# Performance work log

Measured on AMD Instinct MI355X. Metric: run time of the kernel, lower is better.

Reference implementation:

```python
import jax, jax.numpy as jnp
import numpy as np

KNOW, ITEM, D, L, LAT, B, S = 1024, 20000, 128, 2, 256, 256, 200
NTOT = ITEM + KNOW
E1, E2 = 32768, 160000


def graph_layer(h, W, a, src, dst, n):
    # GAT-style: gather src/dst, edge MLP, segment softmax over dst, weighted scatter-sum
    z = h @ W                                              # [N, D]
    e = jax.nn.leaky_relu((jnp.concatenate([z[src], z[dst]], axis=-1) @ a)[:, 0])  # [E]
    m = jax.ops.segment_max(e, dst, num_segments=n)
    m = jnp.where(jnp.isfinite(m), m, 0.0)                 # nodes with no in-edges
    w = jnp.exp(e - m[dst])                                # [E]
    den = jax.ops.segment_sum(w, dst, num_segments=n)      # [N]
    num = jax.ops.segment_sum(w[:, None] * z[src], dst, num_segments=n)  # [N, D]
    return jnp.where(den[:, None] > 0, num / jnp.maximum(den, 1e-12)[:, None], 0.0)


def setup_inputs() -> dict:
    key = jax.random.key(0)
    ks = jax.random.split(key, 32)
    p = lambda i, shp: jax.random.normal(ks[i], shp, dtype=jnp.float32) * 0.05
    inp = {
        'p_rec': jax.random.randint(ks[0], (B, S), 0, ITEM),
        'p_target': jax.random.randint(ks[1], (B,), 0, S),
        'a_rec': jax.random.randint(ks[2], (B, S), 0, 3),
        'kn_rec': jax.random.uniform(ks[3], (B, S, KNOW), dtype=jnp.float32),
        'kn_num': jnp.ones((B, S), dtype=jnp.float32),
        'src1': jax.random.randint(ks[4], (E1,), 0, KNOW),
        'dst1': jax.random.randint(ks[5], (E1,), 0, KNOW),
        'src2': jax.random.randint(ks[6], (E2,), 0, NTOT),
        'dst2': jax.random.randint(ks[7], (E2,), 0, NTOT),
        'src3': jax.random.randint(ks[8], (E2,), 0, NTOT),
        'dst3': jax.random.randint(ks[9], (E2,), 0, NTOT),
        'kn_table': p(10, (KNOW, D)),
        'exer_table': p(11, (ITEM, D)),
        'ans_table': p(12, (3, D)),
        'gW': p(13, (L, 3, D, D)),
        'gA': p(14, (L, 3, 2 * D, 1)),
        'raW1': p(15, (L, D, D)),
        'raB1': jnp.zeros((L, D), jnp.float32),
        'raW2': p(16, (L, D, 1)),
        'actW1': p(17, (3 * D, LAT)),
        'actB1': jnp.zeros((LAT,), jnp.float32),
        'actW2': p(18, (LAT, ITEM)),
        'actB2': jnp.zeros((ITEM,), jnp.float32),
        'vW1': p(19, (3, 3 * D, LAT)),
        'vB1': jnp.zeros((3, LAT), jnp.float32),
        'vW2': p(20, (3, LAT, 1)),
        'vB2': jnp.zeros((3, 1), jnp.float32),
    }
    return inp


def reference(p_rec, p_target, a_rec, kn_rec, kn_num, src1, dst1, src2, dst2, src3, dst3,
              kn_table, exer_table, ans_table, gW, gA, raW1, raB1, raW2,
              actW1, actB1, actW2, actB2, vW1, vB1, vW2, vB2):
    kn, ex = kn_table, exer_table
    for l in range(L):  # GraphEncoder: stacked Fusion blocks (distinct params)
        k_dir = graph_layer(kn, gW[l, 0], gA[l, 0], src1, dst1, KNOW)
        ek = jnp.concatenate([ex, kn], axis=0)             # [NTOT, D]
        kfe = graph_layer(ek, gW[l, 1], gA[l, 1], src2, dst2, NTOT)
        efk = graph_layer(ek, gW[l, 2], gA[l, 2], src3, dst3, NTOT)
        A_, B_ = k_dir, kfe[ITEM:]
        ra = lambda x: jnp.tanh(x @ raW1[l] + raB1[l]) @ raW2[l]  # [KNOW, 1]
        s = jax.nn.softmax(jnp.concatenate([ra(A_), ra(B_)], axis=1), axis=1)
        kn = s[:, :1] * A_ + s[:, 1:2] * B_
        ex = efk[:ITEM]
    # hidden_layer
    be = ex[p_rec]                                         # [B, S, D]
    ba = ans_table[a_rec]                                  # [B, S, D]
    bk = jnp.einsum('bsk,kd->bsd', kn_rec, kn) / kn_num[..., None]
    item = jnp.concatenate([be, ba, bk], axis=-1)          # [B, S, 3D]
    m = (jnp.arange(S)[None, :] < (p_target + 1)[:, None]).astype(item.dtype)
    h = (item * m[..., None]).sum(axis=1) / m.sum(axis=1, keepdims=True)  # [B, 3D]
    logits = jnp.tanh(h @ actW1 + actB1) @ actW2 + actB2   # [B, ITEM]
    vh = jnp.tanh(jnp.einsum('bd,kdl->kbl', h, vW1) + vB1[:, None, :])
    vals = jnp.einsum('kbl,klo->kbo', vh, vW2) + vB2[:, None, :]  # [3, B, 1]
    return logits, vals[0], vals[1], vals[2]
```

## Files before the change

kernel.cpp:

```cpp
#include <hip/hip_runtime.h>

#define D 128
#define KNOW 1024
#define ITEM 20000
#define NTOT (ITEM + KNOW)
#define LAYERS 2
#define LAT 256
#define BB 256
#define SS 200
#define H3 (3 * D)
#define ZROWS 64
#define NBK (KNOW / ZROWS)
#define NBN ((NTOT + ZROWS - 1) / ZROWS)
#define XPITCH 68

__global__ __launch_bounds__(256) void zdv(
    const float* __restrict__ Xe, const float* __restrict__ Xk,
    const float* __restrict__ gW, const float* __restrict__ gA, int layer,
    float* __restrict__ z1, float* __restrict__ z2, float* __restrict__ z3,
    float* __restrict__ ds1, float* __restrict__ dd1,
    float* __restrict__ ds2, float* __restrict__ dd2,
    float* __restrict__ ds3, float* __restrict__ dd3)
{
    __shared__ __align__(16) float xT[D * XPITCH];
    int bid = blockIdx.x;
    int g, row0, nmax;
    if (bid < NBK)            { g = 0; row0 = bid * ZROWS;                nmax = KNOW; }
    else if (bid < NBK + NBN) { g = 1; row0 = (bid - NBK) * ZROWS;        nmax = NTOT; }
    else                      { g = 2; row0 = (bid - NBK - NBN) * ZROWS;  nmax = NTOT; }
    const float* W = gW + (size_t)(layer * 3 + g) * D * D;
    const float* A = gA + (size_t)(layer * 3 + g) * 2 * D;
    float* Z  = (g == 0) ? z1  : (g == 1 ? z2  : z3);
    float* DS = (g == 0) ? ds1 : (g == 1 ? ds2 : ds3);
    float* DD = (g == 0) ? dd1 : (g == 1 ? dd2 : dd3);

    int tid = threadIdx.x;
#pragma unroll
    for (int i = 0; i < 8; ++i) {
        int flat = tid + i * 256;
        int row  = flat >> 5;
        int f4   = flat & 31;
        int grow = row0 + row;
        float4 v = make_float4(0.f, 0.f, 0.f, 0.f);
        if (grow < nmax) {
            const float* src = (g == 0) ? (Xk + (size_t)grow * D)
                             : (grow < ITEM ? Xe + (size_t)grow * D
                                            : Xk + (size_t)(grow - ITEM) * D);
            v = *(const float4*)(src + f4 * 4);
        }
        int slot = row ^ ((f4 & 7) << 2);
        int kk = f4 * 4;
        xT[(kk + 0) * XPITCH + slot] = v.x;
        xT[(kk + 1) * XPITCH + slot] = v.y;
        xT[(kk + 2) * XPITCH + slot] = v.z;
        xT[(kk + 3) * XPITCH + slot] = v.w;
    }
    __syncthreads();

    int cg = tid & 31;
    int rg = tid >> 5;
    int c0 = cg * 4;
    int r0a = rg * 8, r0b = rg * 8 + 4;

    float acc[8][4];
#pragma unroll
    for (int r = 0; r < 8; ++r)
#pragma unroll
        for (int c = 0; c < 4; ++c) acc[r][c] = 0.f;

#pragma unroll 4
    for (int k = 0; k < D; ++k) {
        float4 wv = *(const float4*)(W + (size_t)k * D + c0);
        int xc = ((k >> 2) & 7) << 2;
        float4 xa = *(const float4*)&xT[k * XPITCH + (r0a ^ xc)];
        float4 xb = *(const float4*)&xT[k * XPITCH + (r0b ^ xc)];
        acc[0][0] = fmaf(xa.x, wv.x, acc[0][0]); acc[0][1] = fmaf(xa.x, wv.y, acc[0][1]);
        acc[0][2] = fmaf(xa.x, wv.z, acc[0][2]); acc[0][3] = fmaf(xa.x, wv.w, acc[0][3]);
        acc[1][0] = fmaf(xa.y, wv.x, acc[1][0]); acc[1][1] = fmaf(xa.y, wv.y, acc[1][1]);
        acc[1][2] = fmaf(xa.y, wv.z, acc[1][2]); acc[1][3] = fmaf(xa.y, wv.w, acc[1][3]);
        acc[2][0] = fmaf(xa.z, wv.x, acc[2][0]); acc[2][1] = fmaf(xa.z, wv.y, acc[2][1]);
        acc[2][2] = fmaf(xa.z, wv.z, acc[2][2]); acc[2][3] = fmaf(xa.z, wv.w, acc[2][3]);
        acc[3][0] = fmaf(xa.w, wv.x, acc[3][0]); acc[3][1] = fmaf(xa.w, wv.y, acc[3][1]);
        acc[3][2] = fmaf(xa.w, wv.z, acc[3][2]); acc[3][3] = fmaf(xa.w, wv.w, acc[3][3]);
        acc[4][0] = fmaf(xb.x, wv.x, acc[4][0]); acc[4][1] = fmaf(xb.x, wv.y, acc[4][1]);
        acc[4][2] = fmaf(xb.x, wv.z, acc[4][2]); acc[4][3] = fmaf(xb.x, wv.w, acc[4][3]);
        acc[5][0] = fmaf(xb.y, wv.x, acc[5][0]); acc[5][1] = fmaf(xb.y, wv.y, acc[5][1]);
        acc[5][2] = fmaf(xb.y, wv.z, acc[5][2]); acc[5][3] = fmaf(xb.y, wv.w, acc[5][3]);
        acc[6][0] = fmaf(xb.z, wv.x, acc[6][0]); acc[6][1] = fmaf(xb.z, wv.y, acc[6][1]);
        acc[6][2] = fmaf(xb.z, wv.z, acc[6][2]); acc[6][3] = fmaf(xb.z, wv.w, acc[6][3]);
        acc[7][0] = fmaf(xb.w, wv.x, acc[7][0]); acc[7][1] = fmaf(xb.w, wv.y, acc[7][1]);
        acc[7][2] = fmaf(xb.w, wv.z, acc[7][2]); acc[7][3] = fmaf(xb.w, wv.w, acc[7][3]);
    }

#pragma unroll
    for (int r = 0; r < 8; ++r) {
        int grow = row0 + ((r < 4) ? (r0a + r) : (r0b + r - 4));
        if (grow < nmax) {
            float4 v = make_float4(acc[r][0], acc[r][1], acc[r][2], acc[r][3]);
            *(float4*)(Z + (size_t)grow * D + c0) = v;
        }
    }

    float4 as = *(const float4*)(A + c0);
    float4 ad = *(const float4*)(A + D + c0);
    float ps[8], pd[8];
#pragma unroll
    for (int r = 0; r < 8; ++r) {
        ps[r] = acc[r][0] * as.x + acc[r][1] * as.y + acc[r][2] * as.z + acc[r][3] * as.w;
        pd[r] = acc[r][0] * ad.x + acc[r][1] * ad.y + acc[r][2] * ad.z + acc[r][3] * ad.w;
    }
#pragma unroll
    for (int m = 16; m; m >>= 1) {
#pragma unroll
        for (int r = 0; r < 8; ++r) {
            ps[r] += __shfl_xor(ps[r], m, 64);
            pd[r] += __shfl_xor(pd[r], m, 64);
        }
    }
    if (cg == 0) {
#pragma unroll
        for (int r = 0; r < 8; ++r) {
            int grow = row0 + ((r < 4) ? (r0a + r) : (r0b + r - 4));
            if (grow < nmax) { DS[grow] = ps[r]; DD[grow] = pd[r]; }
        }
    }
}

__global__ void hist3(const int* __restrict__ d1, const int* __restrict__ d2, const int* __restrict__ d3,
                      int E1, int E2, int* __restrict__ c1, int* __restrict__ c2, int* __restrict__ c3) {
    int i = blockIdx.x * blockDim.x + threadIdx.x;
    if (i < E1) atomicAdd(&c1[d1[i]], 1);
    else if (i < E1 + E2) { int d = d2[i - E1]; if (d >= ITEM) atomicAdd(&c2[d - ITEM], 1); }
    else if (i < E1 + 2 * E2) { int d = d3[i - E1 - E2]; if (d < ITEM) atomicAdd(&c3[d], 1); }
}

__global__ __launch_bounds__(1024) void exscan3(int* __restrict__ c1, int* __restrict__ o1,
                                                int* __restrict__ c2, int* __restrict__ o2,
                                                int* __restrict__ c3, int* __restrict__ o3) {
    int g = blockIdx.x;
    int* cnt = (g == 0) ? c1 : (g == 1 ? c2 : c3);
    int* off = (g == 0) ? o1 : (g == 1 ? o2 : o3);
    int n = (g == 2) ? ITEM : KNOW;
    int tid = threadIdx.x, lane = tid & 63, wid = tid >> 6;
    int L = (n + 1023) >> 10;
    int i0 = tid * L;
    int sum = 0;
    for (int q = 0; q < L; ++q) {
        int i = i0 + q;
        if (i < n) sum += cnt[i];
    }
    int x = sum;
#pragma unroll
    for (int d = 1; d < 64; d <<= 1) { int t = __shfl_up(x, d, 64); if (lane >= d) x += t; }
    __shared__ int ws[16];
    if (lane == 63) ws[wid] = x;
    __syncthreads();
    if (wid == 0) {
        int w = (lane < 16) ? ws[lane] : 0;
#pragma unroll
        for (int d = 1; d < 16; d <<= 1) { int t = __shfl_up(w, d, 64); if (lane >= d) w += t; }
        if (lane < 16) ws[lane] = w;
    }
    __syncthreads();
    int run = x - sum + ((wid > 0) ? ws[wid - 1] : 0);
    if (tid == 0) off[0] = 0;
    for (int q = 0; q < L; ++q) {
        int i = i0 + q;
        if (i < n) {
            int v = cnt[i];
            cnt[i] = run;
            run += v;
            off[i + 1] = run;
        }
    }
}

__global__ void scatter3(const int* __restrict__ s1, const int* __restrict__ d1,
                         const int* __restrict__ s2, const int* __restrict__ d2,
                         const int* __restrict__ s3, const int* __restrict__ d3,
                         int E1, int E2, int* __restrict__ cur1, int* __restrict__ cur2, int* __restrict__ cur3,
                         int* __restrict__ e1, int* __restrict__ e2, int* __restrict__ e3) {
    int i = blockIdx.x * blockDim.x + threadIdx.x;
    if (i < E1) { int p = atomicAdd(&cur1[d1[i]], 1); e1[p] = s1[i]; }
    else if (i < E1 + E2) { int j = i - E1; int d = d2[j]; if (d >= ITEM) { int p = atomicAdd(&cur2[d - ITEM], 1); e2[p] = s2[j]; } }
    else if (i < E1 + 2 * E2) { int j = i - E1 - E2; int d = d3[j]; if (d < ITEM) { int p = atomicAdd(&cur3[d], 1); e3[p] = s3[j]; } }
}

__device__ __forceinline__ void agg_row(const float* __restrict__ Z, const float* __restrict__ dsrc,
                                        float dd, const int* __restrict__ es, int e0, int e1,
                                        int lane, float* __restrict__ acc) {
#pragma unroll
    for (int q = 0; q < 8; ++q) acc[q] = 0.f;
    if (e1 <= e0) return;
    float mx = -3.4e38f;
    for (int e = e0 + lane; e < e1; e += 64) {
        float t = dsrc[es[e]] + dd;
        t = (t > 0.f) ? t : 0.01f * t;
        mx = fmaxf(mx, t);
    }
#pragma unroll
    for (int o = 32; o; o >>= 1) mx = fmaxf(mx, __shfl_xor(mx, o, 64));
    int eg = lane >> 4, cs = lane & 15;
    float den = 0.f;
    for (int e = e0 + eg; e < e1; e += 4) {
        int s = es[e];
        float t = dsrc[s] + dd;
        t = (t > 0.f) ? t : 0.01f * t;
        float w = __expf(t - mx);
        den += w;
        const float4* zr = (const float4*)(Z + (size_t)s * D + cs * 8);
        float4 za = zr[0], zb = zr[1];
        acc[0] = fmaf(w, za.x, acc[0]); acc[1] = fmaf(w, za.y, acc[1]);
        acc[2] = fmaf(w, za.z, acc[2]); acc[3] = fmaf(w, za.w, acc[3]);
        acc[4] = fmaf(w, zb.x, acc[4]); acc[5] = fmaf(w, zb.y, acc[5]);
        acc[6] = fmaf(w, zb.z, acc[6]); acc[7] = fmaf(w, zb.w, acc[7]);
    }
#pragma unroll
    for (int m = 16; m <= 32; m <<= 1) {
        den += __shfl_xor(den, m, 64);
#pragma unroll
        for (int q = 0; q < 8; ++q) acc[q] += __shfl_xor(acc[q], m, 64);
    }
    float inv = 1.f / fmaxf(den, 1e-12f);
#pragma unroll
    for (int q = 0; q < 8; ++q) acc[q] *= inv;
}

__global__ __launch_bounds__(256) void agg3c(
    const float* __restrict__ z1, const float* __restrict__ z2, const float* __restrict__ z3,
    const float* __restrict__ ds1, const float* __restrict__ dd1,
    const float* __restrict__ ds2, const float* __restrict__ dd2,
    const float* __restrict__ ds3, const float* __restrict__ dd3,
    const int* __restrict__ off1, const int* __restrict__ es1,
    const int* __restrict__ off2, const int* __restrict__ es2,
    const int* __restrict__ off3, const int* __restrict__ es3,
    const float* __restrict__ raW1, const float* __restrict__ raB1,
    const float* __restrict__ raW2, float* __restrict__ buf)
{
    int wv = threadIdx.x >> 6, lane = threadIdx.x & 63;
    int eg = lane >> 4, cs = lane & 15;
    if (blockIdx.x < KNOW / 4) {
        __shared__ float ABs[4][2][D];
        int i = blockIdx.x * 4 + wv;
        float accA[8], accB[8];
        agg_row(z1, ds1, dd1[i], es1, off1[i], off1[i + 1], lane, accA);
        agg_row(z2, ds2, dd2[ITEM + i], es2, off2[i], off2[i + 1], lane, accB);
        if (eg == 0) {
            *(float4*)&ABs[wv][0][cs * 8]     = make_float4(accA[0], accA[1], accA[2], accA[3]);
            *(float4*)&ABs[wv][0][cs * 8 + 4] = make_float4(accA[4], accA[5], accA[6], accA[7]);
            *(float4*)&ABs[wv][1][cs * 8]     = make_float4(accB[0], accB[1], accB[2], accB[3]);
            *(float4*)&ABs[wv][1][cs * 8 + 4] = make_float4(accB[4], accB[5], accB[6], accB[7]);
        }
        __syncthreads();
        int j0 = lane * 2;
        float b0 = raB1[j0], b1 = raB1[j0 + 1];
        float aA0 = b0, aA1 = b1, aB0 = b0, aB1 = b1;
#pragma unroll 4
        for (int k = 0; k < D; ++k) {
            float av = ABs[wv][0][k], bv = ABs[wv][1][k];
            float2 w = *(const float2*)(raW1 + (size_t)k * D + j0);
            aA0 = fmaf(av, w.x, aA0); aA1 = fmaf(av, w.y, aA1);
            aB0 = fmaf(bv, w.x, aB0); aB1 = fmaf(bv, w.y, aB1);
        }
        float2 w2 = *(const float2*)(raW2 + j0);
        float pA = tanhf(aA0) * w2.x + tanhf(aA1) * w2.y;
        float pB = tanhf(aB0) * w2.x + tanhf(aB1) * w2.y;
#pragma unroll
        for (int o = 32; o; o >>= 1) { pA += __shfl_xor(pA, o, 64); pB += __shfl_xor(pB, o, 64); }
        float mx2 = fmaxf(pA, pB);
        float eA = __expf(pA - mx2), eB = __expf(pB - mx2);
        float s = 1.f / (eA + eB);
        float sA = eA * s, sB = eB * s;
        float2 Av = *(float2*)&ABs[wv][0][j0];
        float2 Bv = *(float2*)&ABs[wv][1][j0];
        *(float2*)(buf + (size_t)(ITEM + i) * D + j0) =
            make_float2(sA * Av.x + sB * Bv.x, sA * Av.y + sB * Bv.y);
    } else {
        int row = (blockIdx.x - KNOW / 4) * 4 + wv;
        if (row < ITEM) {
            float acc[8];
            agg_row(z3, ds3, dd3[row], es3, off3[row], off3[row + 1], lane, acc);
            if (eg == 0) {
                *(float4*)(buf + (size_t)row * D + cs * 8)     = make_float4(acc[0], acc[1], acc[2], acc[3]);
                *(float4*)(buf + (size_t)row * D + cs * 8 + 4) = make_float4(acc[4], acc[5], acc[6], acc[7]);
            }
        }
    }
}

__global__ __launch_bounds__(512) void hker(const float* __restrict__ ex, const float* __restrict__ ans_table,
                                            const int* __restrict__ p_rec, const int* __restrict__ a_rec,
                                            const int* __restrict__ p_target,
                                            const float* __restrict__ kn_rec, const float* __restrict__ kn_num,
                                            const float* __restrict__ kn, float* __restrict__ h) {
    int b = blockIdx.x;
    int tid = threadIdx.x;
    int j = tid & 127, sg = tid >> 7;
    int cnt = p_target[b] + 1;
    __shared__ int pidx[SS], aidx[SS];
    __shared__ float kr[KNOW];
    __shared__ float red[4][3][128];
    for (int i = tid; i < cnt; i += 512) { pidx[i] = p_rec[b * SS + i]; aidx[i] = a_rec[b * SS + i]; }
    {
        float a0 = 0.f, a1 = 0.f;
        const float* kb = kn_rec + (size_t)b * SS * KNOW + tid * 2;
        const float* nb = kn_num + (size_t)b * SS;
#pragma unroll 2
        for (int s = 0; s < cnt; ++s) {
            float inv = 1.f / nb[s];
            float2 v = *(const float2*)(kb + (size_t)s * KNOW);
            a0 = fmaf(v.x, inv, a0); a1 = fmaf(v.y, inv, a1);
        }
        kr[tid * 2] = a0; kr[tid * 2 + 1] = a1;
    }
    __syncthreads();
    float accE = 0.f, accA = 0.f;
    for (int s = sg; s < cnt; s += 4) {
        accE += ex[(size_t)pidx[s] * D + j];
        accA += ans_table[aidx[s] * D + j];
    }
    float accK = 0.f;
    for (int k = sg * 256; k < sg * 256 + 256; ++k) accK += kr[k] * kn[(size_t)k * D + j];
    red[sg][0][j] = accE; red[sg][1][j] = accA; red[sg][2][j] = accK;
    __syncthreads();
    if (sg == 0) {
        float inv = 1.f / (float)cnt;
        float e = (red[0][0][j] + red[1][0][j] + red[2][0][j] + red[3][0][j]) * inv;
        float a = (red[0][1][j] + red[1][1][j] + red[2][1][j] + red[3][1][j]) * inv;
        float kv = (red[0][2][j] + red[1][2][j] + red[2][2][j] + red[3][2][j]) * inv;
        h[b * H3 + j] = e;
        h[b * H3 + D + j] = a;
        h[b * H3 + 2 * D + j] = kv;
    }
}

__global__ __launch_bounds__(256) void hidden_gemm(const float* __restrict__ h,
                                                   const float* __restrict__ actW1, const float* __restrict__ actB1,
                                                   const float* __restrict__ vW1, const float* __restrict__ vB1,
                                                   float* __restrict__ hid) {
    __shared__ float hT[H3 * 17];
    int tid = threadIdx.x;
    int b0 = blockIdx.y * 16;
    for (int idx = tid; idx < 16 * H3; idx += 256) {
        int r = idx / H3, k = idx - r * H3;
        hT[k * 17 + r] = h[(size_t)(b0 + r) * H3 + k];
    }
    __syncthreads();
    int j = blockIdx.x * 64 + (tid & 63);
    int head = j >> 8, jj = j & 255;
    int rg = tid >> 6, r0 = rg * 4;
    const float* W = (head == 0) ? actW1 : (vW1 + (size_t)(head - 1) * H3 * LAT);
    float bias = (head == 0) ? actB1[jj] : vB1[(head - 1) * LAT + jj];
    float acc[4] = {bias, bias, bias, bias};
#pragma unroll 4
    for (int k = 0; k < H3; ++k) {
        float w = W[(size_t)k * LAT + jj];
        float h0 = hT[k * 17 + r0 + 0];
        float h1 = hT[k * 17 + r0 + 1];
        float h2 = hT[k * 17 + r0 + 2];
        float h3 = hT[k * 17 + r0 + 3];
        acc[0] = fmaf(h0, w, acc[0]);
        acc[1] = fmaf(h1, w, acc[1]);
        acc[2] = fmaf(h2, w, acc[2]);
        acc[3] = fmaf(h3, w, acc[3]);
    }
#pragma unroll
    for (int r = 0; r < 4; ++r)
        hid[((size_t)head * BB + (b0 + r0 + r)) * LAT + jj] = tanhf(acc[r]);
}

__global__ __launch_bounds__(256) void logitsker(const float* __restrict__ hid, const float* __restrict__ actW2,
                                                 const float* __restrict__ actB2, float* __restrict__ out) {
    __shared__ float hT[LAT * 33];
    int tid = threadIdx.x;
    int b0 = blockIdx.y * 32;
    for (int idx = tid; idx < 32 * LAT; idx += 256) {
        int r = idx >> 8, k = idx & 255;
        hT[k * 33 + r] = hid[(size_t)(b0 + r) * LAT + k];
    }
    __syncthreads();
    int lane6 = tid & 63;
    int rg = tid >> 6, r0 = rg * 8;
    int ibase = blockIdx.x * 256 + lane6;
    int icol[4], icl[4];
    float bias[4];
#pragma unroll
    for (int c = 0; c < 4; ++c) {
        icol[c] = ibase + c * 64;
        icl[c] = icol[c] < ITEM ? icol[c] : (ITEM - 1);
        bias[c] = actB2[icl[c]];
    }
    float acc[8][4];
#pragma unroll
    for (int r = 0; r < 8; ++r)
#pragma unroll
        for (int c = 0; c < 4; ++c) acc[r][c] = bias[c];
#pragma unroll 2
    for (int k = 0; k < LAT; ++k) {
        float w0 = actW2[(size_t)k * ITEM + icl[0]];
        float w1 = actW2[(size_t)k * ITEM + icl[1]];
        float w2 = actW2[(size_t)k * ITEM + icl[2]];
        float w3 = actW2[(size_t)k * ITEM + icl[3]];
        const float* hp = &hT[k * 33 + r0];
#pragma unroll
        for (int r = 0; r < 8; ++r) {
            float hv = hp[r];
            acc[r][0] = fmaf(hv, w0, acc[r][0]);
            acc[r][1] = fmaf(hv, w1, acc[r][1]);
            acc[r][2] = fmaf(hv, w2, acc[r][2]);
            acc[r][3] = fmaf(hv, w3, acc[r][3]);
        }
    }
#pragma unroll
    for (int c = 0; c < 4; ++c) {
        if (icol[c] < ITEM) {
#pragma unroll
            for (int r = 0; r < 8; ++r)
                out[(size_t)(b0 + r0 + r) * ITEM + icol[c]] = acc[r][c];
        }
    }
}

__global__ __launch_bounds__(256) void valsker(const float* __restrict__ hid, const float* __restrict__ vW2,
                                               const float* __restrict__ vB2, float* __restrict__ out) {
    int idx = blockIdx.x * 4 + (threadIdx.x >> 6);
    int lane = threadIdx.x & 63;
    if (idx >= 3 * BB) return;
    int k = idx / BB, b = idx - k * BB;
    const float* vh = hid + ((size_t)(k + 1) * BB + b) * LAT;
    float4 a = ((const float4*)vh)[lane];
    float4 w = ((const float4*)(vW2 + k * LAT))[lane];
    float s = a.x * w.x + a.y * w.y + a.z * w.z + a.w * w.w;
#pragma unroll
    for (int o = 32; o; o >>= 1) s += __shfl_down(s, o, 64);
    if (lane == 0) out[(size_t)BB * ITEM + k * BB + b] = s + vB2[k];
}

extern "C" void kernel_launch(void* const* d_in, const int* in_sizes, int n_in,
                              void* d_out, int out_size, void* d_ws, size_t ws_size,
                              hipStream_t stream) {
    const int*   p_rec      = (const int*)d_in[0];
    const int*   p_target   = (const int*)d_in[1];
    const int*   a_rec      = (const int*)d_in[2];
    const float* kn_rec     = (const float*)d_in[3];
    const float* kn_num     = (const float*)d_in[4];
    const int*   src1       = (const int*)d_in[5];
    const int*   dst1       = (const int*)d_in[6];
    const int*   src2       = (const int*)d_in[7];
    const int*   dst2       = (const int*)d_in[8];
    const int*   src3       = (const int*)d_in[9];
    const int*   dst3       = (const int*)d_in[10];
    const float* kn_table   = (const float*)d_in[11];
    const float* exer_table = (const float*)d_in[12];
    const float* ans_table  = (const float*)d_in[13];
    const float* gW         = (const float*)d_in[14];
    const float* gA         = (const float*)d_in[15];
    const float* raW1       = (const float*)d_in[16];
    const float* raB1       = (const float*)d_in[17];
    const float* raW2       = (const float*)d_in[18];
    const float* actW1      = (const float*)d_in[19];
    const float* actB1      = (const float*)d_in[20];
    const float* actW2      = (const float*)d_in[21];
    const float* actB2      = (const float*)d_in[22];
    const float* vW1        = (const float*)d_in[23];
    const float* vB1        = (const float*)d_in[24];
    const float* vW2        = (const float*)d_in[25];
    const float* vB2        = (const float*)d_in[26];
    const int E1 = in_sizes[5], E2 = in_sizes[7];

    float* base = (float*)d_ws;
    size_t o = 0;
    auto alloc = [&](size_t n) -> float* { float* p = base + o; o += (n + 3) & ~(size_t)3; return p; };
    float* buf  = alloc((size_t)NTOT * D);
    float* z1   = alloc((size_t)KNOW * D);
    float* z2   = alloc((size_t)NTOT * D);
    float* z3   = alloc((size_t)NTOT * D);
    float* ds1 = alloc(KNOW);  float* dd1 = alloc(KNOW);
    float* ds2 = alloc(NTOT);  float* dd2 = alloc(NTOT);
    float* ds3 = alloc(NTOT);  float* dd3 = alloc(NTOT);
    int* cnts = (int*)alloc(2 * KNOW + NTOT);
    int* cnt1 = cnts, *cnt2 = cnts + KNOW, *cnt3 = cnts + 2 * KNOW;
    int* off1 = (int*)alloc(KNOW + 1);
    int* off2 = (int*)alloc(KNOW + 1);
    int* off3 = (int*)alloc(ITEM + 1);
    int* es1  = (int*)alloc(E1);
    int* es2  = (int*)alloc(E2);
    int* es3  = (int*)alloc(E2);
    float* hbuf  = alloc((size_t)BB * H3);
    float* hid   = alloc((size_t)4 * BB * LAT);

    hipMemsetAsync(cnts, 0, sizeof(int) * (2 * KNOW + NTOT), stream);

    int etot = E1 + 2 * E2;
    hist3<<<(etot + 255) / 256, 256, 0, stream>>>(dst1, dst2, dst3, E1, E2, cnt1, cnt2, cnt3);
    exscan3<<<3, 1024, 0, stream>>>(cnt1, off1, cnt2, off2, cnt3, off3);
    scatter3<<<(etot + 255) / 256, 256, 0, stream>>>(src1, dst1, src2, dst2, src3, dst3,
                                                     E1, E2, cnt1, cnt2, cnt3, es1, es2, es3);

    int aggBlocks = KNOW / 4 + ITEM / 4;
    for (int l = 0; l < LAYERS; ++l) {
        const float* Xe = (l == 0) ? exer_table : buf;
        const float* Xk = (l == 0) ? kn_table : (buf + (size_t)ITEM * D);
        zdv<<<NBK + 2 * NBN, 256, 0, stream>>>(Xe, Xk, gW, gA, l, z1, z2, z3,
                                               ds1, dd1, ds2, dd2, ds3, dd3);
        agg3c<<<aggBlocks, 256, 0, stream>>>(z1, z2, z3, ds1, dd1, ds2, dd2, ds3, dd3,
                                             off1, es1, off2, es2, off3, es3,
                                             raW1 + (size_t)l * D * D, raB1 + (size_t)l * D,
                                             raW2 + (size_t)l * D, buf);
    }

    hker<<<BB, 512, 0, stream>>>(buf, ans_table, p_rec, a_rec, p_target, kn_rec, kn_num,
                                 buf + (size_t)ITEM * D, hbuf);
    hidden_gemm<<<dim3(16, 16), 256, 0, stream>>>(hbuf, actW1, actB1, vW1, vB1, hid);
    logitsker<<<dim3((ITEM + 255) / 256, 8), 256, 0, stream>>>(hid, actW2, actB2, (float*)d_out);
    valsker<<<(3 * BB + 3) / 4, 256, 0, stream>>>(hid, vW2, vB2, (float*)d_out);
}
```

Baseline: 320.9 us.

## Split kn_rec row reduction over sequence chunks into separate kernel

Moves the masked sum of kn_rec/kn_num over the sequence out of hker into a new krowk kernel. krowk runs a BB x CH grid, each block summing one chunk of the sequence with float4 loads and writing a partial row. hker then adds the CH partials. The old loop ran 256 blocks serially over up to 200 rows of the ~200MB kn_rec, so the goal is more memory-level parallelism for that stream, at the cost of an extra launch and 8MB of partial-sum traffic.

```diff
diff --git a/kernel.cpp b/kernel.cpp
--- a/kernel.cpp
+++ b/kernel.cpp
@@ -9,6 +9,7 @@
 #define BB 256
 #define SS 200
 #define H3 (3 * D)
+#define CH 8
 #define ZROWS 64
 #define NBK (KNOW / ZROWS)
 #define NBN ((NTOT + ZROWS - 1) / ZROWS)
@@ -288,30 +289,39 @@
     }
 }
 
+__global__ __launch_bounds__(256) void krowk(const float* __restrict__ kn_rec, const float* __restrict__ kn_num,
+                                             const int* __restrict__ p_target, float* __restrict__ krowP) {
+    int b = blockIdx.x, ch = blockIdx.y;
+    int cnt = p_target[b] + 1;
+    int per = (SS + CH - 1) / CH;
+    int s0 = ch * per, s1 = s0 + per;
+    if (s1 > cnt) s1 = cnt;
+    int k0 = threadIdx.x * 4;
+    float4 a = make_float4(0.f, 0.f, 0.f, 0.f);
+    for (int s = s0; s < s1; ++s) {
+        float inv = 1.f / kn_num[b * SS + s];
+        float4 v = *(const float4*)(kn_rec + ((size_t)b * SS + s) * KNOW + k0);
+        a.x += v.x * inv; a.y += v.y * inv; a.z += v.z * inv; a.w += v.w * inv;
+    }
+    *(float4*)(krowP + ((size_t)ch * BB + b) * KNOW + k0) = a;
+}
+
 __global__ __launch_bounds__(512) void hker(const float* __restrict__ ex, const float* __restrict__ ans_table,
                                             const int* __restrict__ p_rec, const int* __restrict__ a_rec,
-                                            const int* __restrict__ p_target,
-                                            const float* __restrict__ kn_rec, const float* __restrict__ kn_num,
+                                            const int* __restrict__ p_target, const float* __restrict__ krowP,
                                             const float* __restrict__ kn, float* __restrict__ h) {
     int b = blockIdx.x;
-    int tid = threadIdx.x;
-    int j = tid & 127, sg = tid >> 7;
+    int j = threadIdx.x & 127, sg = threadIdx.x >> 7;
     int cnt = p_target[b] + 1;
     __shared__ int pidx[SS], aidx[SS];
     __shared__ float kr[KNOW];
     __shared__ float red[4][3][128];
-    for (int i = tid; i < cnt; i += 512) { pidx[i] = p_rec[b * SS + i]; aidx[i] = a_rec[b * SS + i]; }
-    {
-        float a0 = 0.f, a1 = 0.f;
-        const float* kb = kn_rec + (size_t)b * SS * KNOW + tid * 2;
-        const float* nb = kn_num + (size_t)b * SS;
-#pragma unroll 2
-        for (int s = 0; s < cnt; ++s) {
-            float inv = 1.f / nb[s];
-            float2 v = *(const float2*)(kb + (size_t)s * KNOW);
-            a0 = fmaf(v.x, inv, a0); a1 = fmaf(v.y, inv, a1);
-        }
-        kr[tid * 2] = a0; kr[tid * 2 + 1] = a1;
+    for (int i = threadIdx.x; i < cnt; i += 512) { pidx[i] = p_rec[b * SS + i]; aidx[i] = a_rec[b * SS + i]; }
+    for (int i = threadIdx.x; i < KNOW; i += 512) {
+        float s = 0.f;
+#pragma unroll
+        for (int c = 0; c < CH; ++c) s += krowP[((size_t)c * BB + b) * KNOW + i];
+        kr[i] = s;
     }
     __syncthreads();
     float accE = 0.f, accA = 0.f;
@@ -486,6 +496,7 @@
     int* es1  = (int*)alloc(E1);
     int* es2  = (int*)alloc(E2);
     int* es3  = (int*)alloc(E2);
+    float* krowP = alloc((size_t)CH * BB * KNOW);
     float* hbuf  = alloc((size_t)BB * H3);
     float* hid   = alloc((size_t)4 * BB * LAT);
 
@@ -509,8 +520,8 @@
                                              raW2 + (size_t)l * D, buf);
     }
 
-    hker<<<BB, 512, 0, stream>>>(buf, ans_table, p_rec, a_rec, p_target, kn_rec, kn_num,
-                                 buf + (size_t)ITEM * D, hbuf);
+    krowk<<<dim3(BB, CH), 256, 0, stream>>>(kn_rec, kn_num, p_target, krowP);
+    hker<<<BB, 512, 0, stream>>>(buf, ans_table, p_rec, a_rec, p_target, krowP, buf + (size_t)ITEM * D, hbuf);
     hidden_gemm<<<dim3(16, 16), 256, 0, stream>>>(hbuf, actW1, actB1, vW1, vB1, hid);
     logitsker<<<dim3((ITEM + 255) / 256, 8), 256, 0, stream>>>(hid, actW2, actB2, (float*)d_out);
     valsker<<<(3 * BB + 3) / 4, 256, 0, stream>>>(hid, vW2, vB2, (float*)d_out);
```

Measured after the change: 312.7 us, median of 2. -2.6%, faster.
